# Optimization experiments

Measured on AMD Instinct MI355X. Metric: run time of the kernel, lower is better.

## Reference

```python
import jax, jax.numpy as jnp
import numpy as np

B, T, D, H = 2, 2048, 1024, 16

def setup_inputs() -> dict:
    key = jax.random.key(0)
    k0, k1, k2, k3 = jax.random.split(key, 4)
    s = 0.02
    return {
        "x": jax.random.normal(k0, (B, T, D), dtype=jnp.float32),
        "Wqkv": jax.random.normal(k1, (3 * D, D), dtype=jnp.float32) * s,
        "Wout": jax.random.normal(k2, (D, D), dtype=jnp.float32) * s,
        "bout": jax.random.normal(k3, (D,), dtype=jnp.float32) * s,
    }

def reference(x, Wqkv, Wout, bout):
    b, t, d = x.shape
    h = H
    dh = d // h
    qkv = x @ Wqkv.T  # [b,t,3d]
    q, k, v = jnp.split(qkv, 3, axis=-1)
    def merge_heads(z):
        return z.reshape(b, t, h, dh).transpose(0, 2, 1, 3)  # [b,h,t,dh]
    q, k, v = map(merge_heads, (q, k, v))
    scale = dh ** -0.5
    dots = jnp.einsum('bhid,bhjd->bhij', q, k) * scale  # [b,h,t,t]
    causal_mask = jnp.triu(jnp.ones((t, t), dtype=bool), 1)
    dots = jnp.where(causal_mask, -jnp.inf, dots)
    attn = jax.nn.softmax(dots, axis=-1)
    out = jnp.einsum('bhij,bhjd->bhid', attn, v)  # [b,h,t,dh]
    out = out.transpose(0, 2, 1, 3).reshape(b, t, d)
    return out @ Wout.T + bout
```

## Files before the change

kernel.cpp:

```cpp
#include <hip/hip_runtime.h>
#include <hip/hip_bf16.h>
#include <math.h>

typedef __bf16 bf16x8 __attribute__((ext_vector_type(8)));
typedef float f32x4 __attribute__((ext_vector_type(4)));
typedef unsigned short u16;
typedef unsigned int u32;
typedef u32 u32x4 __attribute__((ext_vector_type(4)));

#define EXP2F(x) __builtin_amdgcn_exp2f(x)

constexpr int Bz = 2, T = 2048, D = 1024, H = 16;
constexpr int M = Bz * T;
constexpr int NQKV = 3 * D;
constexpr float SCALE2 = 0.125f * 1.44269504089f;

#define GLD_LDS16(g, l) __builtin_amdgcn_global_load_lds( \
    (__attribute__((address_space(1))) void*)(g),          \
    (__attribute__((address_space(3))) void*)(l), 16, 0, 0)

__global__ void cvt_all_kernel(const float* __restrict__ x,
                               const float* __restrict__ wq,
                               const float* __restrict__ wo,
                               u16* __restrict__ xb, u16* __restrict__ wqb,
                               u16* __restrict__ wob) {
  constexpr int NX = M * D / 4;
  constexpr int NQ = NQKV * D / 4;
  constexpr int NW = D * D / 4;
  constexpr int TOT = NX + NQ + NW;
  int i = blockIdx.x * blockDim.x + threadIdx.x;
  int stride = gridDim.x * blockDim.x;
  for (; i < TOT; i += stride) {
    const float4* src;
    u16* dst;
    int j;
    if (i < NX) { src = (const float4*)x; dst = xb; j = i; }
    else if (i < NX + NQ) { src = (const float4*)wq; dst = wqb; j = i - NX; }
    else { src = (const float4*)wo; dst = wob; j = i - NX - NQ; }
    float4 f = src[j];
    ushort4 u;
    u.x = __builtin_bit_cast(u16, (__bf16)f.x);
    u.y = __builtin_bit_cast(u16, (__bf16)f.y);
    u.z = __builtin_bit_cast(u16, (__bf16)f.z);
    u.w = __builtin_bit_cast(u16, (__bf16)f.w);
    ((ushort4*)dst)[j] = u;
  }
}

template <bool FP32OUT, bool QSCALE>
__global__ __launch_bounds__(256, 2)
void gemm_bt(const u16* __restrict__ A, const u16* __restrict__ Bm,
             u16* __restrict__ outb, float* __restrict__ outf,
             const float* __restrict__ bias, int K, int ldc) {
  __shared__ __align__(16) u16 sA[128 * 64];
  __shared__ __align__(16) u16 sB[128 * 64];
  const int tid = threadIdx.x;
  const int lane = tid & 63;
  const int wid = tid >> 6;
  const int wr = wid >> 1, wc = wid & 1;

  const int nwg = gridDim.x * gridDim.y;
  const int flat = blockIdx.y * gridDim.x + blockIdx.x;
  const int cpx = nwg >> 3;
  const int swz = (flat & 7) * cpx + (flat >> 3);
  const int bx = swz % gridDim.x;
  const int by = swz / gridDim.x;

  const int row0 = by * 128;
  const int col0 = bx * 128;

  f32x4 acc[4][4];
#pragma unroll
  for (int m = 0; m < 4; ++m)
#pragma unroll
    for (int n = 0; n < 4; ++n) acc[m][n] = (f32x4){0.f, 0.f, 0.f, 0.f};

  const int nk = K >> 6;
  for (int kt = 0; kt < nk; ++kt) {
    const int k0 = kt << 6;
#pragma unroll
    for (int i = 0; i < 4; ++i) {
      int off = i * 4096 + tid * 16;
      int r = off >> 7;
      int cs = (off >> 4) & 7;
      int c = cs ^ (r & 7);
      const u16* ga = A + (size_t)(row0 + r) * K + k0 + c * 8;
      const u16* gb = Bm + (size_t)(col0 + r) * K + k0 + c * 8;
      u16* la = sA + (i * 4096 + (tid & ~63) * 16) / 2;
      u16* lb = sB + (i * 4096 + (tid & ~63) * 16) / 2;
      GLD_LDS16(ga, la);
      GLD_LDS16(gb, lb);
    }
    __syncthreads();
#pragma unroll
    for (int kk = 0; kk < 2; ++kk) {
      bf16x8 af[4], bfv[4];
#pragma unroll
      for (int m = 0; m < 4; ++m) {
        int r = wr * 64 + m * 16 + (lane & 15);
        int cs = (kk * 4 + (lane >> 4)) ^ (r & 7);
        af[m] = *(const bf16x8*)(sA + r * 64 + cs * 8);
      }
#pragma unroll
      for (int n = 0; n < 4; ++n) {
        int r = wc * 64 + n * 16 + (lane & 15);
        int cs = (kk * 4 + (lane >> 4)) ^ (r & 7);
        bfv[n] = *(const bf16x8*)(sB + r * 64 + cs * 8);
      }
#pragma unroll
      for (int m = 0; m < 4; ++m)
#pragma unroll
        for (int n = 0; n < 4; ++n)
          acc[m][n] = __builtin_amdgcn_mfma_f32_16x16x32_bf16(
              af[m], bfv[n], acc[m][n], 0, 0, 0);
    }
    __syncthreads();
  }

  const int orow0 = row0 + wr * 64;
  const int ocol0 = col0 + wc * 64;
#pragma unroll
  for (int m = 0; m < 4; ++m)
#pragma unroll
    for (int n = 0; n < 4; ++n)
#pragma unroll
      for (int j = 0; j < 4; ++j) {
        int rr = orow0 + m * 16 + (lane >> 4) * 4 + j;
        int cc = ocol0 + n * 16 + (lane & 15);
        if (FP32OUT) {
          outf[(size_t)rr * ldc + cc] = acc[m][n][j] + bias[cc];
        } else {
          float v = acc[m][n][j];
          if (QSCALE && cc < D) v *= SCALE2;
          outb[(size_t)rr * ldc + cc] = __builtin_bit_cast(u16, (__bf16)v);
        }
      }
}

__global__ __launch_bounds__(256, 4)
void flash_kernel(const u16* __restrict__ qkv, u16* __restrict__ attn_out) {
  __shared__ __align__(16) u16 sK[2][64 * 64];
  __shared__ __align__(16) u16 sVt[2][64 * 72];

  const int tid = threadIdx.x;
  const int lane = tid & 63;
  const int l15 = lane & 15;
  const int hi = lane >> 4;
  const int w = tid >> 6;
  const int bh = blockIdx.x;
  const int b = bh >> 4, h = bh & 15;

  const int yj = blockIdx.y & 7, yg = blockIdx.y >> 3;
  const int qt = (yg == 0) ? 31 - yj : (yg == 1) ? 16 + yj
               : (yg == 2) ? 15 - yj : yj;
  const int q0 = qt * 64;
  const int nv = qt + 1;

  const size_t base = (size_t)b * T * 3072;
  const u16* qp = qkv + base + 0 * 1024 + h * 64;
  const u16* kp = qkv + base + 1 * 1024 + h * 64;
  const u16* vp = qkv + base + 2 * 1024 + h * 64;

  ushort4 vr[2][2];
  auto stageK = [&](u16* dst, int kt) {
#pragma unroll
    for (int i = 0; i < 2; ++i) {
      int off = i * 4096 + tid * 16;
      int r = off >> 7;
      int cs = (off >> 4) & 7;
      int c = cs ^ (r & 7);
      GLD_LDS16(kp + (size_t)(kt * 64 + r) * 3072 + c * 8,
                dst + (i * 4096 + (tid & ~63) * 16) / 2);
    }
  };
  auto loadV = [&](int kt) {
#pragma unroll
    for (int i = 0; i < 2; ++i) {
      const u16* gsrc = vp + (size_t)(kt * 64 + lane) * 3072 + (i * 4 + w) * 8;
      vr[i][0] = ((const ushort4*)gsrc)[0];
      vr[i][1] = ((const ushort4*)gsrc)[1];
    }
  };
  auto writeV = [&](u16* dst) {
#pragma unroll
    for (int i = 0; i < 2; ++i) {
      int c = i * 4 + w;
      dst[(c * 8 + 0) * 72 + lane] = vr[i][0].x;
      dst[(c * 8 + 1) * 72 + lane] = vr[i][0].y;
      dst[(c * 8 + 2) * 72 + lane] = vr[i][0].z;
      dst[(c * 8 + 3) * 72 + lane] = vr[i][0].w;
      dst[(c * 8 + 4) * 72 + lane] = vr[i][1].x;
      dst[(c * 8 + 5) * 72 + lane] = vr[i][1].y;
      dst[(c * 8 + 6) * 72 + lane] = vr[i][1].z;
      dst[(c * 8 + 7) * 72 + lane] = vr[i][1].w;
    }
  };

  bf16x8 qf[2];
#pragma unroll
  for (int kk = 0; kk < 2; ++kk)
    qf[kk] = *(const bf16x8*)(qp + (size_t)(q0 + w * 16 + l15) * 3072 +
                              kk * 32 + hi * 8);

  f32x4 o_acc[4];
#pragma unroll
  for (int n = 0; n < 4; ++n) o_acc[n] = (f32x4){0.f, 0.f, 0.f, 0.f};
  float m2 = -INFINITY, l_run = 0.f;

  stageK(sK[0], 0);
  loadV(0);
  writeV(sVt[0]);
  __syncthreads();

  const int idxA = l15 + 32 * (hi & 1);
  const int idxB = idxA + 16;
  const bool hiSel = hi >= 2;

  for (int v = 0; v < nv; ++v) {
    const int cur = v & 1;
    const int k0 = v * 64;
    if (v + 1 < nv) {
      stageK(sK[cur ^ 1], v + 1);
      loadV(v + 1);
    }

    bf16x8 kf[2][4];
#pragma unroll
    for (int kk = 0; kk < 2; ++kk)
#pragma unroll
      for (int n = 0; n < 4; ++n) {
        int rk = n * 16 + l15;
        int cs = (kk * 4 + hi) ^ (rk & 7);
        kf[kk][n] = *(const bf16x8*)(&sK[cur][rk * 64 + cs * 8]);
      }

    f32x4 sc[4];
#pragma unroll
    for (int n = 0; n < 4; ++n) sc[n] = (f32x4){0.f, 0.f, 0.f, 0.f};
    __builtin_amdgcn_s_setprio(1);
#pragma unroll
    for (int kk = 0; kk < 2; ++kk)
#pragma unroll
      for (int n = 0; n < 4; ++n)
        sc[n] = __builtin_amdgcn_mfma_f32_16x16x32_bf16(kf[kk][n], qf[kk],
                                                        sc[n], 0, 0, 0);
    __builtin_amdgcn_s_setprio(0);

    const bool diag = (v == nv - 1);
    const int qrow = q0 + w * 16 + l15;
    float mx = -INFINITY;
#pragma unroll
    for (int n = 0; n < 4; ++n)
#pragma unroll
      for (int r = 0; r < 4; ++r) {
        float sv = sc[n][r];
        if (diag) {
          int kpos = k0 + n * 16 + hi * 4 + r;
          if (kpos > qrow) sv = -INFINITY;
        }
        sc[n][r] = sv;
        mx = fmaxf(mx, sv);
      }
    mx = fmaxf(mx, __shfl_xor(mx, 16, 64));
    mx = fmaxf(mx, __shfl_xor(mx, 32, 64));

    const bool skip = __all(mx <= m2);
    float alpha = 1.f;
    if (!skip) {
      float mn = fmaxf(m2, mx);
      alpha = EXP2F(m2 - mn);
      m2 = mn;
    }

    float sum = 0.f;
    u32 pp[4][2];
#pragma unroll
    for (int n = 0; n < 4; ++n) {
      float p0 = EXP2F(sc[n][0] - m2);
      float p1 = EXP2F(sc[n][1] - m2);
      float p2 = EXP2F(sc[n][2] - m2);
      float p3 = EXP2F(sc[n][3] - m2);
      sum += (p0 + p1) + (p2 + p3);
      pp[n][0] = ((u32)__builtin_bit_cast(u16, (__bf16)p1) << 16) |
                 __builtin_bit_cast(u16, (__bf16)p0);
      pp[n][1] = ((u32)__builtin_bit_cast(u16, (__bf16)p3) << 16) |
                 __builtin_bit_cast(u16, (__bf16)p2);
    }
    sum += __shfl_xor(sum, 16, 64);
    sum += __shfl_xor(sum, 32, 64);
    l_run = l_run * alpha + sum;

    bf16x8 pf[2];
#pragma unroll
    for (int ks = 0; ks < 2; ++ks) {
      u32 a0 = __shfl(pp[2 * ks][0], idxA, 64);
      u32 b0 = __shfl(pp[2 * ks + 1][0], idxA, 64);
      u32 a1 = __shfl(pp[2 * ks][1], idxA, 64);
      u32 b1 = __shfl(pp[2 * ks + 1][1], idxA, 64);
      u32 a2 = __shfl(pp[2 * ks][0], idxB, 64);
      u32 b2 = __shfl(pp[2 * ks + 1][0], idxB, 64);
      u32 a3 = __shfl(pp[2 * ks][1], idxB, 64);
      u32 b3 = __shfl(pp[2 * ks + 1][1], idxB, 64);
      u32x4 t;
      t.x = hiSel ? b0 : a0;
      t.y = hiSel ? b1 : a1;
      t.z = hiSel ? b2 : a2;
      t.w = hiSel ? b3 : a3;
      pf[ks] = __builtin_bit_cast(bf16x8, t);
    }

    bf16x8 vf[2][4];
#pragma unroll
    for (int ks = 0; ks < 2; ++ks)
#pragma unroll
      for (int n = 0; n < 4; ++n)
        vf[ks][n] = *(const bf16x8*)(
            &sVt[cur][(n * 16 + l15) * 72 + ks * 32 + hi * 8]);

    if (!skip) {
      float ab[4];
#pragma unroll
      for (int j = 0; j < 4; ++j) ab[j] = __shfl(alpha, hi * 4 + j, 64);
#pragma unroll
      for (int n = 0; n < 4; ++n)
#pragma unroll
        for (int j = 0; j < 4; ++j) o_acc[n][j] *= ab[j];
    }
    __builtin_amdgcn_s_setprio(1);
#pragma unroll
    for (int ks = 0; ks < 2; ++ks)
#pragma unroll
      for (int n = 0; n < 4; ++n)
        o_acc[n] = __builtin_amdgcn_mfma_f32_16x16x32_bf16(pf[ks], vf[ks][n],
                                                           o_acc[n], 0, 0, 0);
    __builtin_amdgcn_s_setprio(0);

    if (v + 1 < nv) writeV(sVt[cur ^ 1]);
    if (v + 1 < nv) __syncthreads();
  }

#pragma unroll
  for (int j = 0; j < 4; ++j) {
    float lj = __shfl(l_run, hi * 4 + j, 64);
    float inv = 1.f / lj;
    int row = q0 + w * 16 + hi * 4 + j;
#pragma unroll
    for (int n = 0; n < 4; ++n) {
      int cc = h * 64 + n * 16 + l15;
      attn_out[((size_t)b * T + row) * 1024 + cc] =
          __builtin_bit_cast(u16, (__bf16)(o_acc[n][j] * inv));
    }
  }
}

extern "C" void kernel_launch(void* const* d_in, const int* in_sizes, int n_in,
                              void* d_out, int out_size, void* d_ws,
                              size_t ws_size, hipStream_t stream) {
  (void)in_sizes; (void)n_in; (void)out_size; (void)ws_size;
  const float* x = (const float*)d_in[0];
  const float* Wqkv = (const float*)d_in[1];
  const float* Wout = (const float*)d_in[2];
  const float* bout = (const float*)d_in[3];
  float* out = (float*)d_out;

  char* ws = (char*)d_ws;
  u16* x_bf = (u16*)(ws + 0);
  u16* wqkv_bf = (u16*)(ws + 8388608);
  u16* wout_bf = (u16*)(ws + 14680064);
  u16* qkvb = (u16*)(ws + 16777216);
  u16* aout = (u16*)(ws + 41943040);

  cvt_all_kernel<<<2048, 256, 0, stream>>>(x, Wqkv, Wout, x_bf, wqkv_bf,
                                           wout_bf);

  gemm_bt<false, true><<<dim3(NQKV / 128, M / 128), 256, 0, stream>>>(
      x_bf, wqkv_bf, qkvb, nullptr, nullptr, D, NQKV);

  flash_kernel<<<dim3(Bz * H, T / 64), 256, 0, stream>>>(qkvb, aout);

  gemm_bt<true, false><<<dim3(D / 128, M / 128), 256, 0, stream>>>(
      aout, wout_bf, nullptr, out, bout, D, D);
}
```

Before: 119.3 us.

## Route P through LDS instead of shuffles and defer row-sum reduction

```diff
diff --git a/kernel.cpp b/kernel.cpp
--- a/kernel.cpp
+++ b/kernel.cpp
@@ -6,7 +6,6 @@
 typedef float f32x4 __attribute__((ext_vector_type(4)));
 typedef unsigned short u16;
 typedef unsigned int u32;
-typedef u32 u32x4 __attribute__((ext_vector_type(4)));
 
 #define EXP2F(x) __builtin_amdgcn_exp2f(x)
 
@@ -137,10 +136,11 @@
       }
 }
 
-__global__ __launch_bounds__(256, 4)
+__global__ __launch_bounds__(256, 3)
 void flash_kernel(const u16* __restrict__ qkv, u16* __restrict__ attn_out) {
   __shared__ __align__(16) u16 sK[2][64 * 64];
   __shared__ __align__(16) u16 sVt[2][64 * 72];
+  __shared__ __align__(16) u16 sP[4][16][72];
 
   const int tid = threadIdx.x;
   const int lane = tid & 63;
@@ -149,10 +149,7 @@
   const int w = tid >> 6;
   const int bh = blockIdx.x;
   const int b = bh >> 4, h = bh & 15;
-
-  const int yj = blockIdx.y & 7, yg = blockIdx.y >> 3;
-  const int qt = (yg == 0) ? 31 - yj : (yg == 1) ? 16 + yj
-               : (yg == 2) ? 15 - yj : yj;
+  const int qt = (gridDim.y - 1) - blockIdx.y;
   const int q0 = qt * 64;
   const int nv = qt + 1;
 
@@ -212,10 +209,6 @@
   writeV(sVt[0]);
   __syncthreads();
 
-  const int idxA = l15 + 32 * (hi & 1);
-  const int idxB = idxA + 16;
-  const bool hiSel = hi >= 2;
-
   for (int v = 0; v < nv; ++v) {
     const int cur = v & 1;
     const int k0 = v * 64;
@@ -233,6 +226,13 @@
         int cs = (kk * 4 + hi) ^ (rk & 7);
         kf[kk][n] = *(const bf16x8*)(&sK[cur][rk * 64 + cs * 8]);
       }
+    bf16x8 vf[2][4];
+#pragma unroll
+    for (int ks = 0; ks < 2; ++ks)
+#pragma unroll
+      for (int n = 0; n < 4; ++n)
+        vf[ks][n] = *(const bf16x8*)(
+            &sVt[cur][(n * 16 + l15) * 72 + ks * 32 + hi * 8]);
 
     f32x4 sc[4];
 #pragma unroll
@@ -273,7 +273,6 @@
     }
 
     float sum = 0.f;
-    u32 pp[4][2];
 #pragma unroll
     for (int n = 0; n < 4; ++n) {
       float p0 = EXP2F(sc[n][0] - m2);
@@ -281,41 +280,14 @@
       float p2 = EXP2F(sc[n][2] - m2);
       float p3 = EXP2F(sc[n][3] - m2);
       sum += (p0 + p1) + (p2 + p3);
-      pp[n][0] = ((u32)__builtin_bit_cast(u16, (__bf16)p1) << 16) |
-                 __builtin_bit_cast(u16, (__bf16)p0);
-      pp[n][1] = ((u32)__builtin_bit_cast(u16, (__bf16)p3) << 16) |
-                 __builtin_bit_cast(u16, (__bf16)p2);
-    }
-    sum += __shfl_xor(sum, 16, 64);
-    sum += __shfl_xor(sum, 32, 64);
+      u32 w01 = ((u32)__builtin_bit_cast(u16, (__bf16)p1) << 16) |
+                __builtin_bit_cast(u16, (__bf16)p0);
+      u32 w23 = ((u32)__builtin_bit_cast(u16, (__bf16)p3) << 16) |
+                __builtin_bit_cast(u16, (__bf16)p2);
+      *(u32*)(&sP[w][l15][n * 16 + hi * 4 + 0]) = w01;
+      *(u32*)(&sP[w][l15][n * 16 + hi * 4 + 2]) = w23;
+    }
     l_run = l_run * alpha + sum;
-
-    bf16x8 pf[2];
-#pragma unroll
-    for (int ks = 0; ks < 2; ++ks) {
-      u32 a0 = __shfl(pp[2 * ks][0], idxA, 64);
-      u32 b0 = __shfl(pp[2 * ks + 1][0], idxA, 64);
-      u32 a1 = __shfl(pp[2 * ks][1], idxA, 64);
-      u32 b1 = __shfl(pp[2 * ks + 1][1], idxA, 64);
-      u32 a2 = __shfl(pp[2 * ks][0], idxB, 64);
-      u32 b2 = __shfl(pp[2 * ks + 1][0], idxB, 64);
-      u32 a3 = __shfl(pp[2 * ks][1], idxB, 64);
-      u32 b3 = __shfl(pp[2 * ks + 1][1], idxB, 64);
-      u32x4 t;
-      t.x = hiSel ? b0 : a0;
-      t.y = hiSel ? b1 : a1;
-      t.z = hiSel ? b2 : a2;
-      t.w = hiSel ? b3 : a3;
-      pf[ks] = __builtin_bit_cast(bf16x8, t);
-    }
-
-    bf16x8 vf[2][4];
-#pragma unroll
-    for (int ks = 0; ks < 2; ++ks)
-#pragma unroll
-      for (int n = 0; n < 4; ++n)
-        vf[ks][n] = *(const bf16x8*)(
-            &sVt[cur][(n * 16 + l15) * 72 + ks * 32 + hi * 8]);
 
     if (!skip) {
       float ab[4];
@@ -328,16 +300,21 @@
     }
     __builtin_amdgcn_s_setprio(1);
 #pragma unroll
-    for (int ks = 0; ks < 2; ++ks)
+    for (int ks = 0; ks < 2; ++ks) {
+      bf16x8 pf = *(const bf16x8*)(&sP[w][l15][ks * 32 + hi * 8]);
 #pragma unroll
       for (int n = 0; n < 4; ++n)
-        o_acc[n] = __builtin_amdgcn_mfma_f32_16x16x32_bf16(pf[ks], vf[ks][n],
+        o_acc[n] = __builtin_amdgcn_mfma_f32_16x16x32_bf16(pf, vf[ks][n],
                                                            o_acc[n], 0, 0, 0);
+    }
     __builtin_amdgcn_s_setprio(0);
 
     if (v + 1 < nv) writeV(sVt[cur ^ 1]);
     if (v + 1 < nv) __syncthreads();
   }
+
+  l_run += __shfl_xor(l_run, 16, 64);
+  l_run += __shfl_xor(l_run, 32, 64);
 
 #pragma unroll
   for (int j = 0; j < 4; ++j) {
```

After: 107.5 us. -9.9%, faster.
